# Kernel tuning notes

Hardware: AMD Instinct MI355X
Metric: run time of the kernel (lower is better)

## Reference

```python
import jax, jax.numpy as jnp
import numpy as np

E = 131072   # total edges
B = 64       # number of graphs
H = 256      # hidden_dim
S = 32       # num_seeds
NH = 8       # num_heads
HD = H // NH # head_dim = 32


def setup_inputs() -> dict:
    key = jax.random.key(0)
    ks = jax.random.split(key, 12)
    edge_features = jax.random.normal(ks[0], (E, H), dtype=jnp.float32)
    edge_coords = jax.random.normal(ks[1], (E, 3), dtype=jnp.float32)
    # sorted segment ids; guarantee every graph has >= 1 edge (original skips empties)
    extra = jax.random.randint(ks[2], (E - B,), 0, B)
    batch = jnp.sort(jnp.concatenate([jnp.arange(B), extra])).astype(jnp.int32)
    sc = 1.0 / np.sqrt(H)
    seed_vectors = jax.random.normal(ks[3], (S, H), dtype=jnp.float32)
    # projection weights stored in (in, out) layout: y = x @ W
    w_q = jax.random.normal(ks[4], (H, H), dtype=jnp.float32) * sc
    w_k = jax.random.normal(ks[5], (H, H), dtype=jnp.float32) * sc
    w_v = jax.random.normal(ks[6], (H, H), dtype=jnp.float32) * sc
    w1 = jax.random.normal(ks[7], (S * H, H), dtype=jnp.float32) / np.sqrt(S * H)
    b1 = jnp.zeros((H,), dtype=jnp.float32)
    w2 = jax.random.normal(ks[8], (H, H), dtype=jnp.float32) * sc
    b2 = jnp.zeros((H,), dtype=jnp.float32)
    return {"edge_features": edge_features, "edge_coords": edge_coords,
            "batch": batch, "seed_vectors": seed_vectors,
            "w_q": w_q, "w_k": w_k, "w_v": w_v,
            "w1": w1, "b1": b1, "w2": w2, "b2": b2}


def reference(edge_features, edge_coords, batch, seed_vectors,
              w_q, w_k, w_v, w1, b1, w2, b2):
    # NOTE: the original concatenates ||edge_coords|| then projects with
    # [eye(H) | zeros(H,1)] -> the coord-norm column is annihilated, so
    # augmented_features == edge_features exactly. edge_coords does not
    # influence the output.
    e = edge_features.shape[0]
    q = (seed_vectors @ w_q).reshape(S, NH, HD)          # [S, NH, HD]
    k = (edge_features @ w_k).reshape(e, NH, HD)          # [E, NH, HD]
    v = (edge_features @ w_v).reshape(e, NH, HD)          # [E, NH, HD]
    scores = jnp.einsum('shd,ehd->esh', q, k) / jnp.asarray(HD ** 0.5, k.dtype)
    # segment-wise (per-graph) stable softmax over the edge axis
    m = jax.ops.segment_max(scores, batch, num_segments=B)      # [B, S, NH]
    ex = jnp.exp(scores - m[batch])                              # [E, S, NH]
    denom = jax.ops.segment_sum(ex, batch, num_segments=B)      # [B, S, NH]
    w = ex / denom[batch]                                        # [E, S, NH]
    # pooled[b,s,h,d] = sum_{e in graph b} w[e,s,h] * v[e,h,d]
    # scan over the (small, fixed) seed axis to avoid an [E,S,NH,HD] blowup
    def pool_seed(_, ws):  # ws: [E, NH]
        return None, jax.ops.segment_sum(ws[:, :, None] * v, batch, num_segments=B)
    _, pooled = jax.lax.scan(pool_seed, None, jnp.moveaxis(w, 1, 0))  # [S, B, NH, HD]
    pooled = jnp.moveaxis(pooled, 0, 1).reshape(B, S * H)             # [B, S*H]
    h1 = jax.nn.silu(pooled @ w1 + b1)                                # [B, H]
    return h1 @ w2 + b2                                               # [B, H]
```

## Files before the change

### kernel.cpp

```cpp
#include <hip/hip_runtime.h>
#include <hip/hip_bf16.h>

#define EE  131072
#define BB  64
#define HH  256
#define SS  32
#define NHD 8
#define HDD 32
#define NCC 256

typedef _Float16 f16;
typedef _Float16 f16x4 __attribute__((ext_vector_type(4)));
typedef float    f32x4 __attribute__((ext_vector_type(4)));
typedef unsigned short u16x8 __attribute__((ext_vector_type(8)));

static __device__ __forceinline__ unsigned short f2h(float x){
  f16 h = (f16)x; unsigned short u; __builtin_memcpy(&u, &h, 2); return u;
}
static __device__ __forceinline__ float h2f(unsigned short u){
  f16 h; __builtin_memcpy(&h, &u, 2); return (float)h;
}
static __device__ __forceinline__ unsigned int pk2(float a, float b){
  return (unsigned int)f2h(a) | ((unsigned int)f2h(b) << 16);
}

__global__ __launch_bounds__(256) void k_seg(const int* __restrict__ batch, int* __restrict__ seg){
  int e = blockIdx.x * 256 + threadIdx.x;
  if (e == 0){ seg[0] = 0; seg[BB] = EE; }
  if (e > 0 && e < EE){
    int b = batch[e];
    if (batch[e-1] != b) seg[b] = e;
  }
}

__global__ __launch_bounds__(256) void k_qproj(const float* __restrict__ seeds,
                                               const float* __restrict__ wq,
                                               float* __restrict__ qf){
  __shared__ float ssh[HH];
  int s = blockIdx.x, t = threadIdx.x;
  ssh[t] = seeds[s*HH + t];
  __syncthreads();
  float acc = 0.f;
  for (int j = 0; j < HH; j++) acc += ssh[j] * wq[j*HH + t];
  qf[s*HH + t] = acc;
}

__global__ __launch_bounds__(256) void k_wsc(const float* __restrict__ qf,
                                             const float* __restrict__ wk,
                                             f16* __restrict__ wsc){
  int c = blockIdx.x, t = threadIdx.x;
  int s = c >> 3, h = c & 7;
  __shared__ float qsh[HDD];
  if (t < HDD) qsh[t] = qf[s*HH + h*HDD + t];
  __syncthreads();
  const float* wrow = wk + (size_t)t*HH + h*HDD;
  float acc = 0.f;
#pragma unroll
  for (int d = 0; d < HDD; d++) acc += qsh[d] * wrow[d];
  wsc[c*HH + t] = (f16)(acc * 0.17677669529663687f);
}

__global__ __launch_bounds__(256) void k_xt(const float* __restrict__ X, f16* __restrict__ Xt){
  __shared__ __align__(16) unsigned char lds[64 * 516 + 16];
  const int e0 = blockIdx.x * 256;
  const int t  = threadIdx.x;
  const int f4 = t & 15, t4 = t >> 4;
  const int jr2 = t >> 5;
  const int c16 = t & 31;

  for (int jt = 0; jt < 4; jt++){
    const int j0 = jt * 64;
    if (jt) __syncthreads();
    unsigned* wbase = (unsigned*)lds;
#pragma unroll
    for (int p = 0; p < 8; p++){
      int e = p*32 + 2*t4;
      const float* s0 = X + (size_t)(e0 + e)*HH + j0 + f4*4;
      float4 a = *(const float4*)s0;
      float4 b = *(const float4*)(s0 + HH);
      int wb = e >> 1;
      wbase[(f4*4+0)*129 + wb] = pk2(a.x, b.x);
      wbase[(f4*4+1)*129 + wb] = pk2(a.y, b.y);
      wbase[(f4*4+2)*129 + wb] = pk2(a.z, b.z);
      wbase[(f4*4+3)*129 + wb] = pk2(a.w, b.w);
    }
    __syncthreads();
    const unsigned* rbase = (const unsigned*)lds;
#pragma unroll
    for (int ji = 0; ji < 8; ji++){
      int j = ji*8 + jr2;
      int w = j*129 + c16*4;
      uint4 v = make_uint4(rbase[w], rbase[w+1], rbase[w+2], rbase[w+3]);
      *(uint4*)(Xt + (size_t)(j0 + j)*EE + e0 + c16*8) = v;
    }
  }
}

__global__ __launch_bounds__(512) void k_gemm1(const f16* __restrict__ wsc,
                                               const float* __restrict__ X,
                                               const int* __restrict__ batch,
                                               f16* __restrict__ Pt,
                                               float* __restrict__ denom){
  __shared__ __align__(16) unsigned char smem[66048];
  int* bsh = (int*)(smem + 65536);
  const int tid = threadIdx.x;
  const int e0 = blockIdx.x * 128;
  if (tid < 128) bsh[tid] = batch[e0 + tid];

  const int lane = tid & 63, wid = tid >> 6;
  const int wm = wid >> 1, wn = wid & 1;
  const int r16 = lane & 15, g = lane >> 4;

  f32x4 acc[4][4];
#pragma unroll
  for (int i = 0; i < 4; i++)
#pragma unroll
    for (int j = 0; j < 4; j++) acc[i][j] = (f32x4){0.f, 0.f, 0.f, 0.f};

  for (int j0 = 0; j0 < HH; j0 += 64){
#pragma unroll
    for (int it = 0; it < 4; it++){
      int idx = tid + it*512;
      int row = idx >> 3, ch = idx & 7;
      uint4 v = *(const uint4*)(wsc + row*HH + j0 + ch*8);
      *(uint4*)(smem + row*128 + ((ch*16) ^ ((row & 7) << 4))) = v;
    }
#pragma unroll
    for (int it = 0; it < 2; it++){
      int idx = tid + it*512;
      int er = idx >> 3, ch = idx & 7;
      const float* src = X + (size_t)(e0 + er)*HH + j0 + ch*8;
      float4 f0 = *(const float4*)src;
      float4 f1 = *(const float4*)(src + 4);
      uint4 hv = make_uint4(pk2(f0.x, f0.y), pk2(f0.z, f0.w), pk2(f1.x, f1.y), pk2(f1.z, f1.w));
      *(uint4*)(smem + 32768 + er*128 + ((ch*16) ^ ((er & 7) << 4))) = hv;
    }
    __syncthreads();
#pragma unroll
    for (int ks = 0; ks < 4; ks++){
      const int kb2 = (ks*16 + g*4) * 2;
      f16x4 af[4], bf[4];
#pragma unroll
      for (int mi = 0; mi < 4; mi++){
        int row = wm*64 + mi*16 + r16;
        af[mi] = *(const f16x4*)(smem + row*128 + (kb2 ^ ((row & 7) << 4)));
      }
#pragma unroll
      for (int ni = 0; ni < 4; ni++){
        int row = wn*64 + ni*16 + r16;
        bf[ni] = *(const f16x4*)(smem + 32768 + row*128 + (kb2 ^ ((row & 7) << 4)));
      }
#pragma unroll
      for (int mi = 0; mi < 4; mi++)
#pragma unroll
        for (int ni = 0; ni < 4; ni++)
          acc[mi][ni] = __builtin_amdgcn_mfma_f32_16x16x16f16(af[mi], bf[ni], acc[mi][ni], 0, 0, 0);
    }
    __syncthreads();
  }

#pragma unroll
  for (int mi = 0; mi < 4; mi++)
#pragma unroll
    for (int ni = 0; ni < 4; ni++)
#pragma unroll
      for (int r = 0; r < 4; r++){
        int row = wm*64 + mi*16 + g*4 + r;
        int col = wn*64 + ni*16 + r16;
        *(unsigned short*)(smem + row*256 + ((col*2) ^ ((row & 7) << 4))) = f2h(acc[mi][ni][r]);
      }
  __syncthreads();

  const int rowc = tid >> 1, half = tid & 1;
  float dsum = 0.f;
  int curb = bsh[half*64];
#pragma unroll
  for (int ch = 0; ch < 8; ch++){
    int ebase = half*64 + ch*8;
    uint4 v = *(const uint4*)(smem + rowc*256 + ((half*128 + ch*16) ^ ((rowc & 7) << 4)));
    u16x8 hv; __builtin_memcpy(&hv, &v, 16);
    float p[8];
#pragma unroll
    for (int i = 0; i < 8; i++){
      p[i] = __expf(h2f(hv[i]) - 4.0f);
      int b = bsh[ebase + i];
      if (b != curb){ atomicAdd(&denom[curb*NCC + rowc], dsum); dsum = 0.f; curb = b; }
      dsum += p[i];
    }
    uint4 o = make_uint4(pk2(p[0], p[1]), pk2(p[2], p[3]), pk2(p[4], p[5]), pk2(p[6], p[7]));
    *(uint4*)(Pt + (size_t)rowc*EE + e0 + ebase) = o;
  }
  atomicAdd(&denom[curb*NCC + rowc], dsum);
}

__global__ __launch_bounds__(512) void k_gemm2(const f16* __restrict__ Pt,
                                               const f16* __restrict__ Xt,
                                               const int* __restrict__ seg,
                                               float* __restrict__ T){
  __shared__ __align__(16) unsigned char smem[32768];
  const int b  = blockIdx.x >> 2;
  const int c0 = ((blockIdx.x >> 1) & 1) * 128;
  const int j0 = (blockIdx.x & 1) * 128;
  const int beg = seg[b], end = seg[b + 1];
  const int kbeg = beg & ~63;
  const int nsteps = (end - kbeg + 63) >> 6;

  const int tid = threadIdx.x;
  const int lane = tid & 63, wid = tid >> 6;
  const int wm = wid >> 2, wn = wid & 3;
  const int r16 = lane & 15, g = lane >> 4;

  f32x4 acc[4][2];
#pragma unroll
  for (int i = 0; i < 4; i++)
#pragma unroll
    for (int j = 0; j < 2; j++) acc[i][j] = (f32x4){0.f, 0.f, 0.f, 0.f};

  for (int st = 0; st < nsteps; st++){
    int kk = kbeg + st*64;
#pragma unroll
    for (int it = 0; it < 2; it++){
      int idx = tid + it*512;
      int cr = idx >> 3, ch = idx & 7;
      int eb = kk + ch*8;
      uint4 v = *(const uint4*)(Pt + (size_t)(c0 + cr)*EE + eb);
      if (eb < beg || eb + 8 > end){
        u16x8 hv; __builtin_memcpy(&hv, &v, 16);
#pragma unroll
        for (int i = 0; i < 8; i++) if (eb + i < beg || eb + i >= end) hv[i] = (unsigned short)0;
        __builtin_memcpy(&v, &hv, 16);
      }
      *(uint4*)(smem + cr*128 + ((ch*16) ^ ((cr & 7) << 4))) = v;
    }
#pragma unroll
    for (int it = 0; it < 2; it++){
      int idx = tid + it*512;
      int jr = idx >> 3, ch = idx & 7;
      uint4 v = *(const uint4*)(Xt + (size_t)(j0 + jr)*EE + kk + ch*8);
      *(uint4*)(smem + 16384 + jr*128 + ((ch*16) ^ ((jr & 7) << 4))) = v;
    }
    __syncthreads();
#pragma unroll
    for (int ks = 0; ks < 4; ks++){
      const int kb2 = (ks*16 + g*4) * 2;
      f16x4 af[4], bf[2];
#pragma unroll
      for (int mi = 0; mi < 4; mi++){
        int row = wm*64 + mi*16 + r16;
        af[mi] = *(const f16x4*)(smem + row*128 + (kb2 ^ ((row & 7) << 4)));
      }
#pragma unroll
      for (int ni = 0; ni < 2; ni++){
        int row = wn*32 + ni*16 + r16;
        bf[ni] = *(const f16x4*)(smem + 16384 + row*128 + (kb2 ^ ((row & 7) << 4)));
      }
#pragma unroll
      for (int mi = 0; mi < 4; mi++)
#pragma unroll
        for (int ni = 0; ni < 2; ni++)
          acc[mi][ni] = __builtin_amdgcn_mfma_f32_16x16x16f16(af[mi], bf[ni], acc[mi][ni], 0, 0, 0);
    }
    __syncthreads();
  }

  float* Tb = T + (size_t)b*NCC*HH;
#pragma unroll
  for (int mi = 0; mi < 4; mi++)
#pragma unroll
    for (int ni = 0; ni < 2; ni++)
#pragma unroll
      for (int r = 0; r < 4; r++){
        int row = c0 + wm*64 + mi*16 + g*4 + r;
        int col = j0 + wn*32 + ni*16 + r16;
        Tb[row*HH + col] = acc[mi][ni][r];
      }
}

__global__ __launch_bounds__(256) void k_pool(const float* __restrict__ T,
                                              const float* __restrict__ wv,
                                              const float* __restrict__ denom,
                                              float* __restrict__ pooled){
  __shared__ float wvsh[256][36];
  __shared__ float Tsh[32][257];
  const int b = blockIdx.x >> 3;
  const int h = blockIdx.x & 7;
  const int t = threadIdx.x;
  const int tr = t >> 3;
  const int tc = (t & 7) * 4;

#pragma unroll
  for (int p = 0; p < 8; p++){
    int j = tr + p*32;
    float4 wvv = *(const float4*)&wv[(size_t)j*HH + h*HDD + tc];
    *(float4*)&wvsh[j][tc] = wvv;
    float4 tv = *(const float4*)&T[((size_t)b*NCC + tr*NHD + h)*HH + tc + p*32];
    Tsh[tr][tc + p*32 + 0] = tv.x;
    Tsh[tr][tc + p*32 + 1] = tv.y;
    Tsh[tr][tc + p*32 + 2] = tv.z;
    Tsh[tr][tc + p*32 + 3] = tv.w;
  }
  __syncthreads();

  const int s = tr, d0 = tc;
  float ax = 0.f, ay = 0.f, az = 0.f, aw = 0.f;
#pragma unroll 4
  for (int j = 0; j < HH; j++){
    float tv = Tsh[s][j];
    float4 w4 = *(const float4*)&wvsh[j][d0];
    ax += tv * w4.x; ay += tv * w4.y; az += tv * w4.z; aw += tv * w4.w;
  }
  float sc = 1.0f / denom[b*NCC + s*NHD + h];
  float4 o = make_float4(ax*sc, ay*sc, az*sc, aw*sc);
  *(float4*)&pooled[(size_t)b*8192 + (size_t)(s*NHD + h)*HDD + d0] = o;
}

__global__ __launch_bounds__(256) void k_mlp1(const float* __restrict__ pooled,
                                              const float* __restrict__ w1,
                                              float* __restrict__ h1pre){
  __shared__ float psh[8][256];
  const int b0 = (blockIdx.x >> 5) * 8;
  const int j0 = (blockIdx.x & 31) * 256;
  const int t = threadIdx.x;
  for (int idx = t; idx < 8*256; idx += 256){
    int bb = idx >> 8, jj = idx & 255;
    psh[bb][jj] = pooled[(size_t)(b0 + bb)*8192 + j0 + jj];
  }
  __syncthreads();
  float acc[8];
#pragma unroll
  for (int i = 0; i < 8; i++) acc[i] = 0.f;
  for (int jj = 0; jj < 256; jj++){
    float w = w1[(size_t)(j0 + jj)*HH + t];
#pragma unroll
    for (int bb = 0; bb < 8; bb++) acc[bb] += psh[bb][jj] * w;
  }
#pragma unroll
  for (int bb = 0; bb < 8; bb++) atomicAdd(&h1pre[(b0 + bb)*HH + t], acc[bb]);
}

__global__ __launch_bounds__(256) void k_mlp2(const float* __restrict__ h1pre,
                                              const float* __restrict__ b1,
                                              const float* __restrict__ w2,
                                              const float* __restrict__ b2,
                                              float* __restrict__ out){
  __shared__ float hsh[HH];
  const int b = blockIdx.x, t = threadIdx.x;
  float x = h1pre[b*HH + t] + b1[t];
  hsh[t] = x / (1.0f + __expf(-x));
  __syncthreads();
  float acc = b2[t];
  for (int j = 0; j < HH; j++) acc += hsh[j] * w2[j*HH + t];
  out[b*HH + t] = acc;
}

extern "C" void kernel_launch(void* const* d_in, const int* in_sizes, int n_in,
                              void* d_out, int out_size, void* d_ws, size_t ws_size,
                              hipStream_t stream) {
  const float* X     = (const float*)d_in[0];
  const int*   batch = (const int*)d_in[2];
  const float* seeds = (const float*)d_in[3];
  const float* wq    = (const float*)d_in[4];
  const float* wk    = (const float*)d_in[5];
  const float* wv    = (const float*)d_in[6];
  const float* w1    = (const float*)d_in[7];
  const float* b1    = (const float*)d_in[8];
  const float* w2    = (const float*)d_in[9];
  const float* b2    = (const float*)d_in[10];
  float* out = (float*)d_out;

  char* ws = (char*)d_ws;
  size_t off = 0;
  auto alloc = [&](size_t bytes) -> void* {
    void* p = ws + off;
    off = (off + bytes + 255) & ~(size_t)255;
    return p;
  };
  f16*   Xt     = (f16*)  alloc((size_t)NCC * EE * 2);
  f16*   Pt     = (f16*)  alloc((size_t)NCC * EE * 2);
  float* T      = (float*)alloc((size_t)BB * NCC * HH * 4);
  float* qf     = (float*)alloc((size_t)SS * HH * 4);
  f16*   wsc    = (f16*)  alloc((size_t)NCC * HH * 2);
  int*   seg    = (int*)  alloc((size_t)(BB + 1) * 4);
  float* denom  = (float*)alloc((size_t)BB * NCC * 4);
  float* pooled = (float*)alloc((size_t)BB * 8192 * 4);
  float* h1pre  = (float*)alloc((size_t)BB * HH * 4);

  hipMemsetAsync(denom, 0, (size_t)BB * NCC * 4, stream);
  hipMemsetAsync(h1pre, 0, (size_t)BB * HH * 4, stream);

  k_seg  <<<EE/256, 256, 0, stream>>>(batch, seg);
  k_qproj<<<SS,     256, 0, stream>>>(seeds, wq, qf);
  k_wsc  <<<NCC,    256, 0, stream>>>(qf, wk, wsc);
  k_xt   <<<EE/256, 256, 0, stream>>>(X, Xt);
  k_gemm1<<<EE/128, 512, 0, stream>>>(wsc, X, batch, Pt, denom);
  k_gemm2<<<BB*4,   512, 0, stream>>>(Pt, Xt, seg, T);
  k_pool <<<BB*NHD, 256, 0, stream>>>(T, wv, denom, pooled);
  k_mlp1 <<<256,    256, 0, stream>>>(pooled, w1, h1pre);
  k_mlp2 <<<BB,     256, 0, stream>>>(h1pre, b1, w2, b2, out);
}
```

Measured before the change: 450.4 us.

## Register-prefetch GEMM tiles, use 16x16x32 MFMA, split-K gemm2 with atomics

Both GEMM kernels now load the next K-tile from global memory into registers while computing the current tile. This removes one barrier per step and hides load latency. The MFMA calls switch from 16x16x16 to 16x16x32 f16 with 8-wide fragments, halving instruction count. k_gemm2 splits each graph's edge range in two across twice as many blocks and accumulates into T with atomics, which adds a memset of T to improve occupancy (256 blocks was under-filling the GPU). The cost is atomic traffic and the extra memset.

After: 445.8 us. About the same (-1.0%).

```diff
diff --git a/kernel.cpp b/kernel.cpp
--- a/kernel.cpp
+++ b/kernel.cpp
@@ -11,6 +11,7 @@
 
 typedef _Float16 f16;
 typedef _Float16 f16x4 __attribute__((ext_vector_type(4)));
+typedef _Float16 f16x8 __attribute__((ext_vector_type(8)));
 typedef float    f32x4 __attribute__((ext_vector_type(4)));
 typedef unsigned short u16x8 __attribute__((ext_vector_type(8)));
 
@@ -22,6 +23,13 @@
 }
 static __device__ __forceinline__ unsigned int pk2(float a, float b){
   return (unsigned int)f2h(a) | ((unsigned int)f2h(b) << 16);
+}
+static __device__ __forceinline__ uint4 maskseg(uint4 v, int eb, int beg, int end){
+  u16x8 hv; __builtin_memcpy(&hv, &v, 16);
+#pragma unroll
+  for (int i = 0; i < 8; i++) if (eb + i < beg || eb + i >= end) hv[i] = (unsigned short)0;
+  __builtin_memcpy(&v, &hv, 16);
+  return v;
 }
 
 __global__ __launch_bounds__(256) void k_seg(const int* __restrict__ batch, int* __restrict__ seg){
@@ -110,6 +118,7 @@
   const int lane = tid & 63, wid = tid >> 6;
   const int wm = wid >> 1, wn = wid & 1;
   const int r16 = lane & 15, g = lane >> 4;
+  const int cr = tid >> 3, ch = tid & 7;
 
   f32x4 acc[4][4];
 #pragma unroll
@@ -117,47 +126,62 @@
 #pragma unroll
     for (int j = 0; j < 4; j++) acc[i][j] = (f32x4){0.f, 0.f, 0.f, 0.f};
 
-  for (int j0 = 0; j0 < HH; j0 += 64){
-#pragma unroll
-    for (int it = 0; it < 4; it++){
-      int idx = tid + it*512;
-      int row = idx >> 3, ch = idx & 7;
-      uint4 v = *(const uint4*)(wsc + row*HH + j0 + ch*8);
-      *(uint4*)(smem + row*128 + ((ch*16) ^ ((row & 7) << 4))) = v;
-    }
-#pragma unroll
-    for (int it = 0; it < 2; it++){
-      int idx = tid + it*512;
-      int er = idx >> 3, ch = idx & 7;
-      const float* src = X + (size_t)(e0 + er)*HH + j0 + ch*8;
-      float4 f0 = *(const float4*)src;
-      float4 f1 = *(const float4*)(src + 4);
-      uint4 hv = make_uint4(pk2(f0.x, f0.y), pk2(f0.z, f0.w), pk2(f1.x, f1.y), pk2(f1.z, f1.w));
-      *(uint4*)(smem + 32768 + er*128 + ((ch*16) ^ ((er & 7) << 4))) = hv;
+  uint4 qa[4];
+  float4 qb[4];
+
+#pragma unroll
+  for (int i = 0; i < 4; i++)
+    qa[i] = *(const uint4*)(wsc + (size_t)(cr + i*64)*HH + 0 + ch*8);
+  {
+    const float* s0 = X + (size_t)(e0 + cr)*HH + 0 + ch*8;
+    const float* s1 = X + (size_t)(e0 + cr + 64)*HH + 0 + ch*8;
+    qb[0] = *(const float4*)s0; qb[1] = *(const float4*)(s0 + 4);
+    qb[2] = *(const float4*)s1; qb[3] = *(const float4*)(s1 + 4);
+  }
+
+  for (int jt = 0; jt < 4; jt++){
+    if (jt) __syncthreads();
+#pragma unroll
+    for (int i = 0; i < 4; i++)
+      *(uint4*)(smem + (cr + i*64)*128 + ((ch*16) ^ ((cr & 7) << 4))) = qa[i];
+    {
+      uint4 h0 = make_uint4(pk2(qb[0].x,qb[0].y), pk2(qb[0].z,qb[0].w), pk2(qb[1].x,qb[1].y), pk2(qb[1].z,qb[1].w));
+      uint4 h1 = make_uint4(pk2(qb[2].x,qb[2].y), pk2(qb[2].z,qb[2].w), pk2(qb[3].x,qb[3].y), pk2(qb[3].z,qb[3].w));
+      *(uint4*)(smem + 32768 + cr*128        + ((ch*16) ^ ((cr & 7) << 4))) = h0;
+      *(uint4*)(smem + 32768 + (cr+64)*128   + ((ch*16) ^ ((cr & 7) << 4))) = h1;
+    }
+    if (jt < 3){
+      int j0 = (jt + 1) * 64;
+#pragma unroll
+      for (int i = 0; i < 4; i++)
+        qa[i] = *(const uint4*)(wsc + (size_t)(cr + i*64)*HH + j0 + ch*8);
+      const float* s0 = X + (size_t)(e0 + cr)*HH + j0 + ch*8;
+      const float* s1 = X + (size_t)(e0 + cr + 64)*HH + j0 + ch*8;
+      qb[0] = *(const float4*)s0; qb[1] = *(const float4*)(s0 + 4);
+      qb[2] = *(const float4*)s1; qb[3] = *(const float4*)(s1 + 4);
     }
     __syncthreads();
 #pragma unroll
-    for (int ks = 0; ks < 4; ks++){
-      const int kb2 = (ks*16 + g*4) * 2;
-      f16x4 af[4], bf[4];
+    for (int ks = 0; ks < 2; ks++){
+      f16x8 af[4], bf[4];
 #pragma unroll
       for (int mi = 0; mi < 4; mi++){
         int row = wm*64 + mi*16 + r16;
-        af[mi] = *(const f16x4*)(smem + row*128 + (kb2 ^ ((row & 7) << 4)));
+        af[mi] = *(const f16x8*)(smem + row*128 + ((((ks*4 + g)*16)) ^ ((row & 7) << 4)));
       }
 #pragma unroll
       for (int ni = 0; ni < 4; ni++){
         int row = wn*64 + ni*16 + r16;
-        bf[ni] = *(const f16x4*)(smem + 32768 + row*128 + (kb2 ^ ((row & 7) << 4)));
+        bf[ni] = *(const f16x8*)(smem + 32768 + row*128 + ((((ks*4 + g)*16)) ^ ((row & 7) << 4)));
       }
 #pragma unroll
       for (int mi = 0; mi < 4; mi++)
 #pragma unroll
         for (int ni = 0; ni < 4; ni++)
-          acc[mi][ni] = __builtin_amdgcn_mfma_f32_16x16x16f16(af[mi], bf[ni], acc[mi][ni], 0, 0, 0);
-    }
-    __syncthreads();
-  }
+          acc[mi][ni] = __builtin_amdgcn_mfma_f32_16x16x32_f16(af[mi], bf[ni], acc[mi][ni], 0, 0, 0);
+    }
+  }
+  __syncthreads();
 
 #pragma unroll
   for (int mi = 0; mi < 4; mi++)
@@ -175,9 +199,9 @@
   float dsum = 0.f;
   int curb = bsh[half*64];
 #pragma unroll
-  for (int ch = 0; ch < 8; ch++){
-    int ebase = half*64 + ch*8;
-    uint4 v = *(const uint4*)(smem + rowc*256 + ((half*128 + ch*16) ^ ((rowc & 7) << 4)));
+  for (int cc = 0; cc < 8; cc++){
+    int ebase = half*64 + cc*8;
+    uint4 v = *(const uint4*)(smem + rowc*256 + ((half*128 + cc*16) ^ ((rowc & 7) << 4)));
     u16x8 hv; __builtin_memcpy(&hv, &v, 16);
     float p[8];
 #pragma unroll
@@ -198,17 +222,25 @@
                                                const int* __restrict__ seg,
                                                float* __restrict__ T){
   __shared__ __align__(16) unsigned char smem[32768];
-  const int b  = blockIdx.x >> 2;
-  const int c0 = ((blockIdx.x >> 1) & 1) * 128;
-  const int j0 = (blockIdx.x & 1) * 128;
+  const int b    = blockIdx.x >> 3;
+  const int quad = (blockIdx.x >> 1) & 3;
+  const int kc   = blockIdx.x & 1;
+  const int c0   = (quad >> 1) * 128;
+  const int j0   = (quad & 1) * 128;
   const int beg = seg[b], end = seg[b + 1];
   const int kbeg = beg & ~63;
-  const int nsteps = (end - kbeg + 63) >> 6;
+  const int nst  = (end - kbeg + 63) >> 6;
+  const int nst0 = (nst + 1) >> 1;
+  const int st_lo = kc ? nst0 : 0;
+  const int st_hi = kc ? nst  : nst0;
 
   const int tid = threadIdx.x;
   const int lane = tid & 63, wid = tid >> 6;
   const int wm = wid >> 2, wn = wid & 3;
   const int r16 = lane & 15, g = lane >> 4;
+  const int cr = tid >> 3, ch = tid & 7;
+
+  if (st_lo >= st_hi) return;
 
   f32x4 acc[4][2];
 #pragma unroll
@@ -216,51 +248,54 @@
 #pragma unroll
     for (int j = 0; j < 2; j++) acc[i][j] = (f32x4){0.f, 0.f, 0.f, 0.f};
 
-  for (int st = 0; st < nsteps; st++){
+  uint4 pa0, pa1, pb0, pb1;
+  {
+    int kk = kbeg + st_lo*64;
+    pa0 = *(const uint4*)(Pt + (size_t)(c0 + cr)*EE      + kk + ch*8);
+    pa1 = *(const uint4*)(Pt + (size_t)(c0 + cr + 64)*EE + kk + ch*8);
+    pb0 = *(const uint4*)(Xt + (size_t)(j0 + cr)*EE      + kk + ch*8);
+    pb1 = *(const uint4*)(Xt + (size_t)(j0 + cr + 64)*EE + kk + ch*8);
+  }
+
+  for (int st = st_lo; st < st_hi; st++){
     int kk = kbeg + st*64;
-#pragma unroll
-    for (int it = 0; it < 2; it++){
-      int idx = tid + it*512;
-      int cr = idx >> 3, ch = idx & 7;
+    if (st > st_lo) __syncthreads();
+    {
       int eb = kk + ch*8;
-      uint4 v = *(const uint4*)(Pt + (size_t)(c0 + cr)*EE + eb);
-      if (eb < beg || eb + 8 > end){
-        u16x8 hv; __builtin_memcpy(&hv, &v, 16);
-#pragma unroll
-        for (int i = 0; i < 8; i++) if (eb + i < beg || eb + i >= end) hv[i] = (unsigned short)0;
-        __builtin_memcpy(&v, &hv, 16);
-      }
-      *(uint4*)(smem + cr*128 + ((ch*16) ^ ((cr & 7) << 4))) = v;
-    }
-#pragma unroll
-    for (int it = 0; it < 2; it++){
-      int idx = tid + it*512;
-      int jr = idx >> 3, ch = idx & 7;
-      uint4 v = *(const uint4*)(Xt + (size_t)(j0 + jr)*EE + kk + ch*8);
-      *(uint4*)(smem + 16384 + jr*128 + ((ch*16) ^ ((jr & 7) << 4))) = v;
+      uint4 va0 = pa0, va1 = pa1;
+      if (eb < beg || eb + 8 > end){ va0 = maskseg(va0, eb, beg, end); va1 = maskseg(va1, eb, beg, end); }
+      *(uint4*)(smem + cr*128        + ((ch*16) ^ ((cr & 7) << 4))) = va0;
+      *(uint4*)(smem + (cr+64)*128   + ((ch*16) ^ ((cr & 7) << 4))) = va1;
+      *(uint4*)(smem + 16384 + cr*128      + ((ch*16) ^ ((cr & 7) << 4))) = pb0;
+      *(uint4*)(smem + 16384 + (cr+64)*128 + ((ch*16) ^ ((cr & 7) << 4))) = pb1;
+    }
+    if (st + 1 < st_hi){
+      int kk2 = kbeg + (st+1)*64;
+      pa0 = *(const uint4*)(Pt + (size_t)(c0 + cr)*EE      + kk2 + ch*8);
+      pa1 = *(const uint4*)(Pt + (size_t)(c0 + cr + 64)*EE + kk2 + ch*8);
+      pb0 = *(const uint4*)(Xt + (size_t)(j0 + cr)*EE      + kk2 + ch*8);
+      pb1 = *(const uint4*)(Xt + (size_t)(j0 + cr + 64)*EE + kk2 + ch*8);
     }
     __syncthreads();
 #pragma unroll
-    for (int ks = 0; ks < 4; ks++){
-      const int kb2 = (ks*16 + g*4) * 2;
-      f16x4 af[4], bf[2];
+    for (int ks = 0; ks < 2; ks++){
+      f16x8 af[4], bf[2];
 #pragma unroll
       for (int mi = 0; mi < 4; mi++){
         int row = wm*64 + mi*16 + r16;
-        af[mi] = *(const f16x4*)(smem + row*128 + (kb2 ^ ((row & 7) << 4)));
+        af[mi] = *(const f16x8*)(smem + row*128 + ((((ks*4 + g)*16)) ^ ((row & 7) << 4)));
       }
 #pragma unroll
       for (int ni = 0; ni < 2; ni++){
         int row = wn*32 + ni*16 + r16;
-        bf[ni] = *(const f16x4*)(smem + 16384 + row*128 + (kb2 ^ ((row & 7) << 4)));
+        bf[ni] = *(const f16x8*)(smem + 16384 + row*128 + ((((ks*4 + g)*16)) ^ ((row & 7) << 4)));
       }
 #pragma unroll
       for (int mi = 0; mi < 4; mi++)
 #pragma unroll
         for (int ni = 0; ni < 2; ni++)
-          acc[mi][ni] = __builtin_amdgcn_mfma_f32_16x16x16f16(af[mi], bf[ni], acc[mi][ni], 0, 0, 0);
-    }
-    __syncthreads();
+          acc[mi][ni] = __builtin_amdgcn_mfma_f32_16x16x32_f16(af[mi], bf[ni], acc[mi][ni], 0, 0, 0);
+    }
   }
 
   float* Tb = T + (size_t)b*NCC*HH;
@@ -272,7 +307,7 @@
       for (int r = 0; r < 4; r++){
         int row = c0 + wm*64 + mi*16 + g*4 + r;
         int col = j0 + wn*32 + ni*16 + r16;
-        Tb[row*HH + col] = acc[mi][ni][r];
+        atomicAdd(&Tb[row*HH + col], acc[mi][ni][r]);
       }
 }
 
@@ -387,13 +422,14 @@
 
   hipMemsetAsync(denom, 0, (size_t)BB * NCC * 4, stream);
   hipMemsetAsync(h1pre, 0, (size_t)BB * HH * 4, stream);
+  hipMemsetAsync(T,     0, (size_t)BB * NCC * HH * 4, stream);
 
   k_seg  <<<EE/256, 256, 0, stream>>>(batch, seg);
   k_qproj<<<SS,     256, 0, stream>>>(seeds, wq, qf);
   k_wsc  <<<NCC,    256, 0, stream>>>(qf, wk, wsc);
   k_xt   <<<EE/256, 256, 0, stream>>>(X, Xt);
   k_gemm1<<<EE/128, 512, 0, stream>>>(wsc, X, batch, Pt, denom);
-  k_gemm2<<<BB*4,   512, 0, stream>>>(Pt, Xt, seg, T);
+  k_gemm2<<<BB*8,   512, 0, stream>>>(Pt, Xt, seg, T);
   k_pool <<<BB*NHD, 256, 0, stream>>>(T, wv, denom, pooled);
   k_mlp1 <<<256,    256, 0, stream>>>(pooled, w1, h1pre);
   k_mlp2 <<<BB,     256, 0, stream>>>(h1pre, b1, w2, b2, out);
```
